# Kernel optimization log

Hardware: AMD Instinct MI355X
Metric: run time of the kernel (lower is better)

Reference implementation:

```python
import jax, jax.numpy as jnp
import numpy as np

N_NODES = 100000
N_EDGES = 3200000
N_GRAPHS = 4096
IN_CH = 128
HID = 128


def setup_inputs() -> dict:
    key = jax.random.key(0)
    ks = jax.random.split(key, 16)
    x = jax.random.normal(ks[0], (N_NODES, IN_CH), dtype=jnp.float32)
    edge_index = jax.random.randint(ks[1], (2, N_EDGES), 0, N_NODES, dtype=jnp.int64)
    batch = jnp.sort(jax.random.randint(ks[2], (N_NODES,), 0, N_GRAPHS, dtype=jnp.int64))
    def lin(k, fan_in, fan_out):
        bound = 1.0 / np.sqrt(fan_in)
        kw, kb = jax.random.split(k)
        W = jax.random.uniform(kw, (fan_in, fan_out), minval=-bound, maxval=bound, dtype=jnp.float32)
        b = jax.random.uniform(kb, (fan_out,), minval=-bound, maxval=bound, dtype=jnp.float32)
        return W, b
    W1, b1 = lin(ks[3], IN_CH, HID)
    W2, b2 = lin(ks[4], HID, HID)
    W3, b3 = lin(ks[5], HID, HID)
    lw1, lb1 = lin(ks[6], HID, HID // 2)
    lw2, lb2 = lin(ks[7], HID // 2, 1)
    return {"x": x, "edge_index": edge_index, "batch": batch,
            "W1": W1, "b1": b1, "W2": W2, "b2": b2, "W3": W3, "b3": b3,
            "lw1": lw1, "lb1": lb1, "lw2": lw2, "lb2": lb2}


def _gcn_conv(x, src, dst, norm, W, b, n_nodes):
    h = x @ W                              # [N, out]
    msg = h[src] * norm[:, None]           # gather + scale  [E+N, out]
    agg = jax.ops.segment_sum(msg, dst, num_segments=n_nodes)  # scatter-add
    return agg + b


def reference(x, edge_index, batch, W1, b1, W2, b2, W3, b3, lw1, lb1, lw2, lb2):
    n = x.shape[0]
    loop = jnp.arange(n, dtype=edge_index.dtype)
    src = jnp.concatenate([edge_index[0], loop])   # self-loops appended
    dst = jnp.concatenate([edge_index[1], loop])
    deg = jax.ops.segment_sum(jnp.ones_like(dst, dtype=x.dtype), dst, num_segments=n)
    dinv = deg ** -0.5                              # deg >= 1 due to self-loops
    norm = dinv[src] * dinv[dst]                    # symmetric normalization

    h = x
    for W, b in ((W1, b1), (W2, b2), (W3, b3)):
        h = jax.nn.relu(_gcn_conv(h, src, dst, norm, W, b, n))
        # dropout is identity in eval mode

    # global mean pool over graphs
    sums = jax.ops.segment_sum(h, batch, num_segments=N_GRAPHS)
    counts = jax.ops.segment_sum(jnp.ones((n,), dtype=h.dtype), batch, num_segments=N_GRAPHS)
    pooled = sums / jnp.maximum(counts, 1.0)[:, None]   # [G, HID]

    out = jax.nn.relu(pooled @ lw1 + lb1)
    out = out @ lw2 + lb2
    return out[:, 0]
```

## Files before the change

### kernel.cpp

```cpp
#include <hip/hip_runtime.h>


constexpr int HID = 128;
constexpr int BIN_SHIFT = 8;
constexpr int MAXBINS = 512;
constexpr int CAP_SHIFT = 14;

typedef float f32x4 __attribute__((ext_vector_type(4)));
typedef short short8 __attribute__((ext_vector_type(8)));

static __device__ __forceinline__ unsigned bf16rne(float f) {
    unsigned u = __float_as_uint(f);
    return (u + 0x7FFFu + ((u >> 16) & 1u)) >> 16;
}
static __device__ __forceinline__ unsigned packbf16(float lo, float hi) {
    return bf16rne(lo) | (bf16rne(hi) << 16);
}
static __device__ __forceinline__ float blo(unsigned u) { return __uint_as_float(u << 16); }
static __device__ __forceinline__ float bhi(unsigned u) { return __uint_as_float(u & 0xFFFF0000u); }

__global__ __launch_bounds__(256) void k_initcur(int* __restrict__ bin_cur, int nbins) {
    int b = blockIdx.x * 256 + threadIdx.x;
    if (b < nbins) bin_cur[b] = b << CAP_SHIFT;
}

__global__ __launch_bounds__(256) void k_stage(const int* __restrict__ src,
                                               const int* __restrict__ dst,
                                               int* __restrict__ bin_cursor,
                                               unsigned* __restrict__ staged,
                                               int nE, int nbins) {
    __shared__ int hist[MAXBINS];
    __shared__ int wbase[MAXBINS];
    __shared__ int rank[MAXBINS];
    const int tid = threadIdx.x;
    const long long e0 = (long long)blockIdx.x * 4096;
    int es[16], ed[16];
#pragma unroll
    for (int k = 0; k < 16; ++k) {
        long long e = e0 + k * 256 + tid;
        if (e < nE) { es[k] = src[e]; ed[k] = dst[e]; }
        else        { es[k] = 0; ed[k] = -1; }
    }
    for (int t = tid; t < nbins; t += 256) { hist[t] = 0; rank[t] = 0; }
    __syncthreads();
#pragma unroll
    for (int k = 0; k < 16; ++k)
        if (ed[k] >= 0) atomicAdd(&hist[ed[k] >> BIN_SHIFT], 1);
    __syncthreads();
    for (int t = tid; t < nbins; t += 256)
        wbase[t] = hist[t] ? atomicAdd(&bin_cursor[t], hist[t]) : 0;
    __syncthreads();
#pragma unroll
    for (int k = 0; k < 16; ++k)
        if (ed[k] >= 0) {
            int b = ed[k] >> BIN_SHIFT;
            int r = atomicAdd(&rank[b], 1);
            int w = wbase[b] + r;
            if (w < ((b + 1) << CAP_SHIFT))
                staged[w] = ((unsigned)(ed[k] & ((1 << BIN_SHIFT) - 1)) << 24) | (unsigned)es[k];
        }
}

__global__ __launch_bounds__(256) void k_place2(const int* __restrict__ bin_cur,
                                                const unsigned* __restrict__ staged,
                                                int* __restrict__ esrc,
                                                int* __restrict__ row_start,
                                                int* __restrict__ row_end,
                                                float* __restrict__ dinv, int nN) {
    __shared__ int cnt[1 << BIN_SHIFT];
    __shared__ int sc[1 << BIN_SHIFT];
    const int b = blockIdx.x;
    const int tid = threadIdx.x;
    const int d0 = b << BIN_SHIFT;
    const int dend = min(d0 + (1 << BIN_SHIFT), nN);
    const int p0 = b << CAP_SHIFT;
    const int p1 = bin_cur[b];
    cnt[tid] = 0;
    __syncthreads();
    for (int i = p0 + tid; i < p1; i += 256)
        atomicAdd(&cnt[staged[i] >> 24], 1);
    __syncthreads();
    const int my = cnt[tid];
    sc[tid] = my;
    __syncthreads();
    for (int off = 1; off < 256; off <<= 1) {
        int v = (tid >= off) ? sc[tid - off] : 0;
        __syncthreads();
        sc[tid] += v;
        __syncthreads();
    }
    const int excl = sc[tid] - my;
    const int d = d0 + tid;
    if (d < dend) {
        row_start[d] = p0 + excl;
        row_end[d]   = p0 + excl + my;
        dinv[d] = rsqrtf((float)my + 1.0f);
    }
    __syncthreads();
    cnt[tid] = p0 + excl;
    __syncthreads();
    for (int i = p0 + tid; i < p1; i += 256) {
        unsigned pr = staged[i];
        int pos = atomicAdd(&cnt[pr >> 24], 1);
        esrc[pos] = (int)(pr & 0xFFFFFFu);
    }
}

template <bool A_F32>
__global__ __launch_bounds__(256) void k_gemm_mfma(const void* __restrict__ Aptr,
                                                   const float* __restrict__ W,
                                                   const float* __restrict__ dinv,
                                                   unsigned* __restrict__ h16, int n) {
    __shared__ unsigned lds[128 * 68];
    const int tid  = threadIdx.x;
    const int lane = tid & 63;
    const int w    = tid >> 6;
    const int colb = lane & 15;
    const int kg   = lane >> 4;
    const int row0 = blockIdx.x * 64;

    for (int it = 0; it < 32; ++it) {
        int f = it * 256 + tid;
        int c = f & 127, k2 = f >> 7;
        float w0 = W[(size_t)(2 * k2) * HID + c];
        float w1 = W[(size_t)(2 * k2 + 1) * HID + c];
        lds[c * 68 + k2] = packbf16(w0, w1);
    }

    const int r = row0 + w * 16 + colb;
    uint4 a[4] = {};
    if (r < n) {
        if constexpr (A_F32) {
            const float* A = (const float*)Aptr;
#pragma unroll
            for (int kc = 0; kc < 4; ++kc) {
                const float* p = A + (size_t)r * HID + kc * 32 + kg * 8;
                float4 f0 = *(const float4*)(p);
                float4 f1 = *(const float4*)(p + 4);
                a[kc].x = packbf16(f0.x, f0.y);
                a[kc].y = packbf16(f0.z, f0.w);
                a[kc].z = packbf16(f1.x, f1.y);
                a[kc].w = packbf16(f1.z, f1.w);
            }
        } else {
            const unsigned* A16 = (const unsigned*)Aptr;
#pragma unroll
            for (int kc = 0; kc < 4; ++kc)
                a[kc] = *(const uint4*)(A16 + (size_t)r * 64 + kc * 16 + kg * 4);
        }
    }
    __syncthreads();

    f32x4 acc[8] = {};
#pragma unroll
    for (int ct = 0; ct < 8; ++ct) {
#pragma unroll
        for (int kc = 0; kc < 4; ++kc) {
            uint4 bu = *(const uint4*)&lds[(ct * 16 + colb) * 68 + kc * 16 + kg * 4];
            acc[ct] = __builtin_amdgcn_mfma_f32_16x16x32_bf16(
                __builtin_bit_cast(short8, a[kc]),
                __builtin_bit_cast(short8, bu),
                acc[ct], 0, 0, 0);
        }
    }

    __syncthreads();
    float* Cb = (float*)lds;
#pragma unroll
    for (int ct = 0; ct < 8; ++ct)
#pragma unroll
        for (int reg = 0; reg < 4; ++reg)
            Cb[(w * 16 + kg * 4 + reg) * 132 + ct * 16 + colb] = acc[ct][reg];
    __syncthreads();
    for (int it = 0; it < 16; ++it) {
        int f = it * 256 + tid;
        int rl = f >> 6, cw = f & 63;
        int gr = row0 + rl;
        if (gr < n) {
            float di = dinv[gr];
            float2 v = *(const float2*)&Cb[rl * 132 + 2 * cw];
            h16[(size_t)gr * 64 + cw] = packbf16(v.x * di, v.y * di);
        }
    }
}

__global__ __launch_bounds__(256) void k_agg16(const int* __restrict__ row_start,
                                               const int* __restrict__ row_end,
                                               const int* __restrict__ esrc,
                                               const float* __restrict__ dinv,
                                               const unsigned* __restrict__ h16,
                                               const float* __restrict__ bias,
                                               unsigned* __restrict__ out16, int n,
                                               float* __restrict__ pool_sums,
                                               const int* __restrict__ batch) {
    int t = blockIdx.x * 256 + threadIdx.x;
    int node = t >> 6;
    if (node >= n) return;
    const int lane = t & 63;
    int e0 = row_start[node], e1 = row_end[node];
    e0 = __builtin_amdgcn_readfirstlane(e0);
    e1 = __builtin_amdgcn_readfirstlane(e1);
    float dd = dinv[node];

    unsigned su = h16[(size_t)node * 64 + lane];
    float ax = blo(su), ay = bhi(su);

    int e = e0;
    for (; e + 4 <= e1; e += 4) {
        int s0 = __builtin_amdgcn_readfirstlane(esrc[e + 0]);
        int s1 = __builtin_amdgcn_readfirstlane(esrc[e + 1]);
        int s2 = __builtin_amdgcn_readfirstlane(esrc[e + 2]);
        int s3 = __builtin_amdgcn_readfirstlane(esrc[e + 3]);
        unsigned u0 = h16[(size_t)s0 * 64 + lane];
        unsigned u1 = h16[(size_t)s1 * 64 + lane];
        unsigned u2 = h16[(size_t)s2 * 64 + lane];
        unsigned u3 = h16[(size_t)s3 * 64 + lane];
        ax += blo(u0) + blo(u1) + blo(u2) + blo(u3);
        ay += bhi(u0) + bhi(u1) + bhi(u2) + bhi(u3);
    }
    for (; e < e1; ++e) {
        int s = __builtin_amdgcn_readfirstlane(esrc[e]);
        unsigned u = h16[(size_t)s * 64 + lane];
        ax += blo(u);
        ay += bhi(u);
    }

    const float2 bv = *(const float2*)(bias + 2 * lane);
    float ox = fmaxf(ax * dd + bv.x, 0.f);
    float oy = fmaxf(ay * dd + bv.y, 0.f);
    if (out16) {
        out16[(size_t)node * 64 + lane] = packbf16(ox, oy);
    } else {
        float* p = &pool_sums[(size_t)batch[node] * HID + 2 * lane];
        atomicAdd(p, ox);
        atomicAdd(p + 1, oy);
    }
}

__global__ __launch_bounds__(256) void k_count(const int* __restrict__ batch,
                                               float* __restrict__ cnt, int n) {
    int i = blockIdx.x * 256 + threadIdx.x;
    if (i < n) atomicAdd(&cnt[batch[i]], 1.0f);
}

__global__ __launch_bounds__(64) void k_mlp(const float* __restrict__ sums,
                                            const float* __restrict__ cnt,
                                            const float* __restrict__ lw1,
                                            const float* __restrict__ lb1,
                                            const float* __restrict__ lw2,
                                            const float* __restrict__ lb2,
                                            float* __restrict__ out) {
    int g = blockIdx.x;
    int j = threadIdx.x;
    float inv = 1.0f / fmaxf(cnt[g], 1.0f);
    const float* srow = sums + (size_t)g * HID;
    float acc = lb1[j];
#pragma unroll 8
    for (int k = 0; k < HID; ++k) acc += srow[k] * inv * lw1[k * 64 + j];
    acc = fmaxf(acc, 0.0f);
    float prod = acc * lw2[j];
#pragma unroll
    for (int off = 32; off > 0; off >>= 1) prod += __shfl_down(prod, off);
    if (j == 0) out[g] = prod + lb2[0];
}

extern "C" void kernel_launch(void* const* d_in, const int* in_sizes, int n_in,
                              void* d_out, int out_size, void* d_ws, size_t ws_size,
                              hipStream_t stream) {
    const float* x   = (const float*)d_in[0];
    const int*   ei  = (const int*)d_in[1];
    const int*   bat = (const int*)d_in[2];
    const float* W1  = (const float*)d_in[3];
    const float* b1  = (const float*)d_in[4];
    const float* W2  = (const float*)d_in[5];
    const float* b2  = (const float*)d_in[6];
    const float* W3  = (const float*)d_in[7];
    const float* b3  = (const float*)d_in[8];
    const float* lw1 = (const float*)d_in[9];
    const float* lb1 = (const float*)d_in[10];
    const float* lw2 = (const float*)d_in[11];
    const float* lb2 = (const float*)d_in[12];
    float* out = (float*)d_out;

    const int nN = in_sizes[2];
    const int nE = in_sizes[1] / 2;
    const int G  = out_size;
    const int* src = ei;
    const int* dst = ei + nE;

    const int nbins = (nN + (1 << BIN_SHIFT) - 1) >> BIN_SHIFT;
    const size_t capTotal = (size_t)nbins << CAP_SHIFT;

    char* p = (char*)d_ws;
    auto alloc = [&](size_t bytes) { char* r = p; p += (bytes + 255) & ~(size_t)255; return r; };
    unsigned* act16     = (unsigned*)alloc(sizeof(unsigned) * (size_t)nN * 64);
    unsigned* h16       = (unsigned*)alloc(sizeof(unsigned) * ((size_t)nN * 64 > capTotal ? (size_t)nN * 64 : capTotal));
    float*    dinv      = (float*)alloc(sizeof(float) * nN);
    float*    sums      = (float*)alloc(sizeof(float) * (size_t)G * HID);
    float*    cnt       = (float*)alloc(sizeof(float) * G);
    int*      bin_cur   = (int*)alloc(sizeof(int) * (nbins + 1));
    int*      row_start = (int*)alloc(sizeof(int) * nN);
    int*      row_end   = (int*)alloc(sizeof(int) * nN);
    int*      esrc      = (int*)alloc(sizeof(int) * capTotal);
    unsigned* staged    = (unsigned*)h16;

    const int gemmGrid = (nN + 63) / 64;
    const int aggGrid  = (int)(((long long)nN * 64 + 255) / 256);
    const int edgeWGs  = (int)(((long long)nE + 4095) / 4096);

    k_initcur<<<(nbins + 255) / 256, 256, 0, stream>>>(bin_cur, nbins);
    k_stage<<<edgeWGs, 256, 0, stream>>>(src, dst, bin_cur, staged, nE, nbins);
    k_place2<<<nbins, 256, 0, stream>>>(bin_cur, staged, esrc, row_start, row_end, dinv, nN);

    hipMemsetAsync(sums, 0, sizeof(float) * ((size_t)G * HID + G), stream);
    k_count<<<(nN + 255) / 256, 256, 0, stream>>>(bat, cnt, nN);

    k_gemm_mfma<true ><<<gemmGrid, 256, 0, stream>>>(x, W1, dinv, h16, nN);
    k_agg16<<<aggGrid, 256, 0, stream>>>(row_start, row_end, esrc, dinv, h16, b1, act16, nN, nullptr, nullptr);
    k_gemm_mfma<false><<<gemmGrid, 256, 0, stream>>>(act16, W2, dinv, h16, nN);
    k_agg16<<<aggGrid, 256, 0, stream>>>(row_start, row_end, esrc, dinv, h16, b2, act16, nN, nullptr, nullptr);
    k_gemm_mfma<false><<<gemmGrid, 256, 0, stream>>>(act16, W3, dinv, h16, nN);
    k_agg16<<<aggGrid, 256, 0, stream>>>(row_start, row_end, esrc, dinv, h16, b3, nullptr, nN, sums, bat);

    k_mlp<<<G, 64, 0, stream>>>(sums, cnt, lw1, lb1, lw2, lb2, out);
}
```

Measured before the change: 513.4 us.

## Split aggregation feature halves across XCD groups with two nodes per wavefront

The aggregation kernel now handles each node row as two 32-lane halves, so each wavefront processes two nodes. Blocks are mapped so that XCDs 0-3 process the first 64 channels and XCDs 4-7 the second 64 channels of the same node groups. This is meant to halve the per-XCD L2 working set of the gathered h16 rows and improve cache hit rate on random neighbour gathers. In exchange, edge indices are read twice (once per half) and become non-uniform per wavefront, and the two nodes in a wavefront can have different degrees, which causes divergence.

New measurement: 605.8 us. 1.18x slower.

```diff
diff --git a/kernel.cpp b/kernel.cpp
--- a/kernel.cpp
+++ b/kernel.cpp
@@ -184,54 +184,55 @@
     }
 }
 
-__global__ __launch_bounds__(256) void k_agg16(const int* __restrict__ row_start,
-                                               const int* __restrict__ row_end,
-                                               const int* __restrict__ esrc,
-                                               const float* __restrict__ dinv,
-                                               const unsigned* __restrict__ h16,
-                                               const float* __restrict__ bias,
-                                               unsigned* __restrict__ out16, int n,
-                                               float* __restrict__ pool_sums,
-                                               const int* __restrict__ batch) {
-    int t = blockIdx.x * 256 + threadIdx.x;
-    int node = t >> 6;
+__global__ __launch_bounds__(256) void k_agg16h(const int* __restrict__ row_start,
+                                                const int* __restrict__ row_end,
+                                                const int* __restrict__ esrc,
+                                                const float* __restrict__ dinv,
+                                                const unsigned* __restrict__ h16,
+                                                const float* __restrict__ bias,
+                                                unsigned* __restrict__ out16, int n,
+                                                float* __restrict__ pool_sums,
+                                                const int* __restrict__ batch) {
+    const int bid  = blockIdx.x;
+    const int xcd  = bid & 7;
+    const int half = xcd >> 2;
+    const int g    = ((bid >> 3) << 2) + (xcd & 3);
+    const int w    = threadIdx.x >> 6;
+    const int lane = threadIdx.x & 63;
+    const int node = g * 8 + w * 2 + (lane >> 5);
     if (node >= n) return;
-    const int lane = t & 63;
+    const int ch = (lane & 31) + half * 32;
+
     int e0 = row_start[node], e1 = row_end[node];
-    e0 = __builtin_amdgcn_readfirstlane(e0);
-    e1 = __builtin_amdgcn_readfirstlane(e1);
     float dd = dinv[node];
 
-    unsigned su = h16[(size_t)node * 64 + lane];
+    unsigned su = h16[(size_t)node * 64 + ch];
     float ax = blo(su), ay = bhi(su);
 
     int e = e0;
     for (; e + 4 <= e1; e += 4) {
-        int s0 = __builtin_amdgcn_readfirstlane(esrc[e + 0]);
-        int s1 = __builtin_amdgcn_readfirstlane(esrc[e + 1]);
-        int s2 = __builtin_amdgcn_readfirstlane(esrc[e + 2]);
-        int s3 = __builtin_amdgcn_readfirstlane(esrc[e + 3]);
-        unsigned u0 = h16[(size_t)s0 * 64 + lane];
-        unsigned u1 = h16[(size_t)s1 * 64 + lane];
-        unsigned u2 = h16[(size_t)s2 * 64 + lane];
-        unsigned u3 = h16[(size_t)s3 * 64 + lane];
+        int s0 = esrc[e + 0], s1 = esrc[e + 1], s2 = esrc[e + 2], s3 = esrc[e + 3];
+        unsigned u0 = h16[(size_t)s0 * 64 + ch];
+        unsigned u1 = h16[(size_t)s1 * 64 + ch];
+        unsigned u2 = h16[(size_t)s2 * 64 + ch];
+        unsigned u3 = h16[(size_t)s3 * 64 + ch];
         ax += blo(u0) + blo(u1) + blo(u2) + blo(u3);
         ay += bhi(u0) + bhi(u1) + bhi(u2) + bhi(u3);
     }
     for (; e < e1; ++e) {
-        int s = __builtin_amdgcn_readfirstlane(esrc[e]);
-        unsigned u = h16[(size_t)s * 64 + lane];
+        int s = esrc[e];
+        unsigned u = h16[(size_t)s * 64 + ch];
         ax += blo(u);
         ay += bhi(u);
     }
 
-    const float2 bv = *(const float2*)(bias + 2 * lane);
+    const float2 bv = *(const float2*)(bias + 2 * ch);
     float ox = fmaxf(ax * dd + bv.x, 0.f);
     float oy = fmaxf(ay * dd + bv.y, 0.f);
     if (out16) {
-        out16[(size_t)node * 64 + lane] = packbf16(ox, oy);
+        out16[(size_t)node * 64 + ch] = packbf16(ox, oy);
     } else {
-        float* p = &pool_sums[(size_t)batch[node] * HID + 2 * lane];
+        float* p = &pool_sums[(size_t)batch[node] * HID + 2 * ch];
         atomicAdd(p, ox);
         atomicAdd(p + 1, oy);
     }
@@ -305,8 +306,9 @@
     unsigned* staged    = (unsigned*)h16;
 
     const int gemmGrid = (nN + 63) / 64;
-    const int aggGrid  = (int)(((long long)nN * 64 + 255) / 256);
     const int edgeWGs  = (int)(((long long)nE + 4095) / 4096);
+    const int ngroups  = (((nN + 7) / 8 + 3) / 4) * 4;
+    const int aggGrid  = ngroups * 2;
 
     k_initcur<<<(nbins + 255) / 256, 256, 0, stream>>>(bin_cur, nbins);
     k_stage<<<edgeWGs, 256, 0, stream>>>(src, dst, bin_cur, staged, nE, nbins);
@@ -316,11 +318,11 @@
     k_count<<<(nN + 255) / 256, 256, 0, stream>>>(bat, cnt, nN);
 
     k_gemm_mfma<true ><<<gemmGrid, 256, 0, stream>>>(x, W1, dinv, h16, nN);
-    k_agg16<<<aggGrid, 256, 0, stream>>>(row_start, row_end, esrc, dinv, h16, b1, act16, nN, nullptr, nullptr);
+    k_agg16h<<<aggGrid, 256, 0, stream>>>(row_start, row_end, esrc, dinv, h16, b1, act16, nN, nullptr, nullptr);
     k_gemm_mfma<false><<<gemmGrid, 256, 0, stream>>>(act16, W2, dinv, h16, nN);
-    k_agg16<<<aggGrid, 256, 0, stream>>>(row_start, row_end, esrc, dinv, h16, b2, act16, nN, nullptr, nullptr);
+    k_agg16h<<<aggGrid, 256, 0, stream>>>(row_start, row_end, esrc, dinv, h16, b2, act16, nN, nullptr, nullptr);
     k_gemm_mfma<false><<<gemmGrid, 256, 0, stream>>>(act16, W3, dinv, h16, nN);
-    k_agg16<<<aggGrid, 256, 0, stream>>>(row_start, row_end, esrc, dinv, h16, b3, nullptr, nN, sums, bat);
+    k_agg16h<<<aggGrid, 256, 0, stream>>>(row_start, row_end, esrc, dinv, h16, b3, nullptr, nN, sums, bat);
 
     k_mlp<<<G, 64, 0, stream>>>(sums, cnt, lw1, lb1, lw2, lb2, out);
 }
```
